# Kernel optimization log

Measured on AMD Instinct MI355X. Metric: run time of the kernel, lower is better.

## Reference

```python
import jax, jax.numpy as jnp
import numpy as np

B, N, HID, H = 2, 2048, 2048, 16
DH = HID // H  # 128


def _rope_tables(n, d, base=10000.0):
    inv_freq = 1.0 / (base ** (np.arange(0, d, 2, dtype=np.float32) / d))
    t = np.arange(n, dtype=np.float32)
    freqs = np.outer(t, inv_freq)                 # [N, d/2]
    emb = np.concatenate([freqs, freqs], axis=-1)  # [N, d]
    return jnp.asarray(np.cos(emb)), jnp.asarray(np.sin(emb))


def setup_inputs() -> dict:
    key = jax.random.key(0)
    k1, k2, k3 = jax.random.split(key, 3)
    std = 1.0 / HID ** 0.5
    cos, sin = _rope_tables(N, DH)
    return {
        "hidden_states": jax.random.normal(k1, (B, N, HID), dtype=jnp.float32),
        "cos": cos,
        "sin": sin,
        "w_qkv": (jax.random.truncated_normal(k2, -2.0, 2.0, (3 * HID, HID), jnp.float32) * std),
        "w_o": (jax.random.truncated_normal(k3, -2.0, 2.0, (HID, HID), jnp.float32) * std),
    }


def _rotate_half(x):
    d = x.shape[-1] // 2
    return jnp.concatenate([-x[..., d:], x[..., :d]], axis=-1)


def reference(hidden_states, cos, sin, w_qkv, w_o):
    b, n, _ = hidden_states.shape
    qkv = (hidden_states @ w_qkv.T).reshape(b, n, 3, H, DH)
    q, k, v = qkv[:, :, 0], qkv[:, :, 1], qkv[:, :, 2]  # [B,N,H,DH]
    c = cos[:, None, :]  # [N,1,DH] broadcasts over heads
    s = sin[:, None, :]
    q = q * c + _rotate_half(q) * s
    k = k * c + _rotate_half(k) * s
    scale = 1.0 / jnp.sqrt(jnp.asarray(DH, q.dtype))
    scores = jnp.einsum("bqhd,bkhd->bhqk", q, k) * scale
    attn = jax.nn.softmax(scores, axis=-1)
    out = jnp.einsum("bhqk,bkhd->bqhd", attn, v).reshape(b, n, HID)
    return out @ w_o.T
```

## Files before the change

kernel.cpp:

```cpp
#include <hip/hip_runtime.h>
#include <math.h>

#define NB 2
#define NN 2048
#define HIDDEN 2048
#define NHEAD 16
#define DHEAD 128

typedef __attribute__((ext_vector_type(8))) short bf16x8;
typedef __attribute__((ext_vector_type(4))) float floatx4;

static __device__ __forceinline__ short f2bf(float f) {
    union { float f; unsigned u; } v; v.f = f;
    unsigned r = v.u + 0x7fffu + ((v.u >> 16) & 1u);
    return (short)(r >> 16);
}
static __device__ __forceinline__ void gload_lds16(const short* g, short* l) {
    __builtin_amdgcn_global_load_lds(
        (const __attribute__((address_space(1))) void*)g,
        (__attribute__((address_space(3))) void*)l, 16, 0, 0);
}

__global__ __launch_bounds__(256) void cast_bf16_3(
    const float* __restrict__ a, const float* __restrict__ b, const float* __restrict__ c,
    short* __restrict__ oa, short* __restrict__ ob, short* __restrict__ oc,
    int n4a, int n4b, int n4c)
{
    int i = blockIdx.x * 256 + threadIdx.x;
    const float* s; short* d; int j;
    if (i < n4a) { s = a; d = oa; j = i; }
    else if (i < n4a + n4b) { s = b; d = ob; j = i - n4a; }
    else if (i < n4a + n4b + n4c) { s = c; d = oc; j = i - n4a - n4b; }
    else return;
    float4 v = ((const float4*)s)[j];
    short4 o;
    o.x = f2bf(v.x); o.y = f2bf(v.y); o.z = f2bf(v.z); o.w = f2bf(v.w);
    ((short4*)d)[j] = o;
}

__global__ __launch_bounds__(512, 2) void gemm_qkv_256(
    const short* __restrict__ A, const short* __restrict__ Bw,
    const float* __restrict__ cosT, const float* __restrict__ sinT,
    short* __restrict__ Qp, short* __restrict__ Kp, short* __restrict__ Vtp)
{
    __shared__ __align__(16) short AB[65536];

    const int tid = threadIdx.x;
    const int w = tid >> 6;
    const int l = tid & 63;
    const int quad = l >> 4;
    const int l15 = l & 15;
    const int wr = w >> 2;
    const int wc = w & 3;
    const int bm = blockIdx.y * 256;
    const int bn = blockIdx.x * 256;
    const int K = HIDDEN;

    const short* src[8];
    int ldst[8];
#pragma unroll
    for (int ld = 0; ld < 2; ++ld) {
        int chunk = ld * 512 + tid;
        int row = chunk >> 3;
        int j = (chunk & 7) ^ (row & 7);
        int coff = j * 8;
        int dbase = chunk * 16;
        src[0 * 2 + ld] = Bw + (size_t)(bn + row) * K + coff;
        src[1 * 2 + ld] = A  + (size_t)(bm + row) * K + coff;
        src[2 * 2 + ld] = A  + (size_t)(bm + 128 + row) * K + coff;
        src[3 * 2 + ld] = Bw + (size_t)(bn + 128 + row) * K + coff;
        ldst[0 * 2 + ld] = 32768 + dbase;
        ldst[1 * 2 + ld] = 0 + dbase;
        ldst[2 * 2 + ld] = 16384 + dbase;
        ldst[3 * 2 + ld] = 32768 + 16384 + dbase;
    }

    const int xj = l15 & 7;
    const int jq0 = ((0 * 4 + quad) ^ xj) * 16;
    const int jq1 = ((1 * 4 + quad) ^ xj) * 16;
    const int arow = (wr * 128 + l15) * 128;
    const int brow = (wc * 16 + l15) * 128;

    floatx4 acc[8][4];
#pragma unroll
    for (int i = 0; i < 8; ++i)
#pragma unroll
        for (int j = 0; j < 4; ++j) acc[i][j] = (floatx4){0.f, 0.f, 0.f, 0.f};

#pragma unroll
    for (int i = 0; i < 8; ++i)
        gload_lds16(src[i], (short*)((char*)AB + ldst[i]));

#define STAGE(i) gload_lds16(src[i] + kpf, (short*)((char*)AB + ldst[i] + so))
#define MFMA(d, x, y) d = __builtin_amdgcn_mfma_f32_16x16x32_bf16(x, y, d, 0, 0, 0)

    const int NT = K / 64;
#pragma unroll 1
    for (int t = 0; t < NT; ++t) {
        const int co = (t & 1) << 16;
        const int so = co ^ 65536;
        int kpf = (t + 1) * 64;
        if (kpf == K) kpf = 0;

        bf16x8 a[4][2], b0[2][2], b1[2][2];

        asm volatile("s_waitcnt vmcnt(2)" ::: "memory");
        __builtin_amdgcn_s_barrier();
#pragma unroll
        for (int m = 0; m < 4; ++m) {
            a[m][0] = *(const bf16x8*)((const char*)AB + co + arow + m * 2048 + jq0);
            a[m][1] = *(const bf16x8*)((const char*)AB + co + arow + m * 2048 + jq1);
        }
#pragma unroll
        for (int n = 0; n < 2; ++n) {
            b0[n][0] = *(const bf16x8*)((const char*)AB + co + 32768 + brow + n * 8192 + jq0);
            b0[n][1] = *(const bf16x8*)((const char*)AB + co + 32768 + brow + n * 8192 + jq1);
        }
        STAGE(0); STAGE(1);
        __builtin_amdgcn_s_setprio(1);
#pragma unroll
        for (int m = 0; m < 4; ++m)
#pragma unroll
            for (int n = 0; n < 2; ++n) {
                MFMA(acc[m][n], a[m][0], b0[n][0]);
                MFMA(acc[m][n], a[m][1], b0[n][1]);
            }
        __builtin_amdgcn_s_setprio(0);

        asm volatile("s_waitcnt vmcnt(2)" ::: "memory");
        __builtin_amdgcn_s_barrier();
#pragma unroll
        for (int n = 0; n < 2; ++n) {
            b1[n][0] = *(const bf16x8*)((const char*)AB + co + 32768 + 16384 + brow + n * 8192 + jq0);
            b1[n][1] = *(const bf16x8*)((const char*)AB + co + 32768 + 16384 + brow + n * 8192 + jq1);
        }
        STAGE(2); STAGE(3);
        __builtin_amdgcn_s_setprio(1);
#pragma unroll
        for (int m = 0; m < 4; ++m)
#pragma unroll
            for (int n = 0; n < 2; ++n) {
                MFMA(acc[m][2 + n], a[m][0], b1[n][0]);
                MFMA(acc[m][2 + n], a[m][1], b1[n][1]);
            }
        __builtin_amdgcn_s_setprio(0);

        __builtin_amdgcn_s_barrier();
#pragma unroll
        for (int m = 0; m < 4; ++m) {
            a[m][0] = *(const bf16x8*)((const char*)AB + co + arow + (4 + m) * 2048 + jq0);
            a[m][1] = *(const bf16x8*)((const char*)AB + co + arow + (4 + m) * 2048 + jq1);
        }
        STAGE(4); STAGE(5);
        __builtin_amdgcn_s_setprio(1);
#pragma unroll
        for (int m = 0; m < 4; ++m)
#pragma unroll
            for (int n = 0; n < 2; ++n) {
                MFMA(acc[4 + m][2 + n], a[m][0], b1[n][0]);
                MFMA(acc[4 + m][2 + n], a[m][1], b1[n][1]);
            }
        __builtin_amdgcn_s_setprio(0);

        __builtin_amdgcn_s_barrier();
        STAGE(6); STAGE(7);
        __builtin_amdgcn_s_setprio(1);
#pragma unroll
        for (int m = 0; m < 4; ++m)
#pragma unroll
            for (int n = 0; n < 2; ++n) {
                MFMA(acc[4 + m][n], a[m][0], b0[n][0]);
                MFMA(acc[4 + m][n], a[m][1], b0[n][1]);
            }
        __builtin_amdgcn_s_setprio(0);
    }
#undef STAGE
#undef MFMA

    asm volatile("s_waitcnt vmcnt(0)" ::: "memory");

    const int bx = blockIdx.x;
    const int which = bx >> 3;
    const int hpair = (bx & 7) * 2;
    const float qsc = (which == 0) ? 0.12751791525f : 1.0f;

#pragma unroll
    for (int m = 0; m < 8; ++m) {
#pragma unroll
        for (int reg = 0; reg < 4; ++reg) {
            int gm = bm + wr * 128 + m * 16 + quad * 4 + reg;
            int b = gm >> 11, nseq = gm & (NN - 1);
            if (which == 2) {
#pragma unroll
                for (int n = 0; n < 4; ++n) {
                    int bh = b * NHEAD + hpair + (n >> 1);
                    int d = (n & 1) * 64 + wc * 16 + l15;
                    Vtp[((size_t)bh * DHEAD + d) * NN + nseq] = f2bf(acc[m][n][reg]);
                }
            } else {
                int d0 = wc * 16 + l15;
                float c = cosT[(size_t)nseq * DHEAD + d0];
                float s = sinT[(size_t)nseq * DHEAD + d0];
#pragma unroll
                for (int hb = 0; hb < 2; ++hb) {
                    int bh = b * NHEAD + hpair + hb;
                    short* dst = (which == 0 ? Qp : Kp) + ((size_t)bh * NN + nseq) * DHEAD;
                    float e0 = acc[m][hb * 2 + 0][reg];
                    float e1 = acc[m][hb * 2 + 1][reg];
                    dst[d0]      = f2bf((e0 * c - e1 * s) * qsc);
                    dst[d0 + 64] = f2bf((e1 * c + e0 * s) * qsc);
                }
            }
        }
    }
}

template <int MODE>
__global__ __launch_bounds__(256) void gemm_bf16_nt(
    const short* __restrict__ A, const short* __restrict__ Bw,
    const float* __restrict__ cosT, const float* __restrict__ sinT,
    short* __restrict__ Qp, short* __restrict__ Kp, short* __restrict__ Vtp,
    float* __restrict__ Cp, int M, int N, int K)
{
    __shared__ __align__(16) short AB[1280 * 8];

    const int tid = threadIdx.x;
    const int w = tid >> 6;
    const int l = tid & 63;
    const int quad = l >> 4;
    const int l15 = l & 15;
    const int bm = blockIdx.y * 128;
    const int bn = blockIdx.x * 128;

    const int wm = (w & 1) * 64;
    const int wn2 = w >> 1;

    const short* gptr[5];
    short* lptr[5];
#pragma unroll
    for (int r5 = 0; r5 < 5; ++r5) {
        int s = r5 * 256 + tid;
        int m = (s < 640) ? s : s - 640;
        int row = m / 5;
        int ch = m - row * 5;
        if (ch == 4) ch = 0;
        gptr[r5] = ((s < 640) ? (A + (size_t)(bm + row) * K)
                              : (Bw + (size_t)(bn + row) * K)) + ch * 8;
        lptr[r5] = &AB[s * 8];
    }

    floatx4 acc[4][4];
#pragma unroll
    for (int i = 0; i < 4; ++i)
#pragma unroll
        for (int j = 0; j < 4; ++j) acc[i][j] = (floatx4){0.f, 0.f, 0.f, 0.f};

    for (int k0 = 0; k0 < K; k0 += 32) {
        __syncthreads();
#pragma unroll
        for (int r5 = 0; r5 < 5; ++r5)
            gload_lds16(gptr[r5] + k0, lptr[r5]);
        __syncthreads();

        bf16x8 af[4], bf[4];
#pragma unroll
        for (int i = 0; i < 4; ++i)
            af[i] = *(const bf16x8*)&AB[((wm + i * 16 + l15) * 5 + quad) * 8];
#pragma unroll
        for (int j = 0; j < 4; ++j) {
            int col = wn2 * 32 + (j & 1) * 16 + ((j >> 1) << 6);
            bf[j] = *(const bf16x8*)&AB[(640 + (col + l15) * 5 + quad) * 8];
        }
#pragma unroll
        for (int i = 0; i < 4; ++i)
#pragma unroll
            for (int j = 0; j < 4; ++j)
                acc[i][j] = __builtin_amdgcn_mfma_f32_16x16x32_bf16(af[i], bf[j], acc[i][j], 0, 0, 0);
    }

    if (MODE == 1) {
#pragma unroll
        for (int i = 0; i < 4; ++i) {
#pragma unroll
            for (int reg = 0; reg < 4; ++reg) {
                int row = bm + wm + i * 16 + quad * 4 + reg;
                float* crow = Cp + (size_t)row * N + bn;
#pragma unroll
                for (int j = 0; j < 4; ++j)
                    crow[wn2 * 32 + (j & 1) * 16 + ((j >> 1) << 6) + l15] = acc[i][j][reg];
            }
        }
    } else {
        const int which = bn >> 11;
        const int head = (bn >> 7) & (NHEAD - 1);
        const float qsc = (which == 0) ? 0.12751791525f : 1.0f;
#pragma unroll
        for (int i = 0; i < 4; ++i) {
#pragma unroll
            for (int reg = 0; reg < 4; ++reg) {
                int m = bm + wm + i * 16 + quad * 4 + reg;
                int b = m >> 11, n = m & (NN - 1);
                int bh = b * NHEAD + head;
                if (which == 2) {
#pragma unroll
                    for (int j = 0; j < 4; ++j) {
                        int d = wn2 * 32 + (j & 1) * 16 + ((j >> 1) << 6) + l15;
                        Vtp[((size_t)bh * DHEAD + d) * NN + n] = f2bf(acc[i][j][reg]);
                    }
                } else {
                    short* dst = (which == 0 ? Qp : Kp) + ((size_t)bh * NN + n) * DHEAD;
#pragma unroll
                    for (int j = 0; j < 2; ++j) {
                        int d0 = wn2 * 32 + j * 16 + l15;
                        float c = cosT[(size_t)n * DHEAD + d0];
                        float s = sinT[(size_t)n * DHEAD + d0];
                        float e0 = acc[i][j][reg], e1 = acc[i][j + 2][reg];
                        dst[d0]      = f2bf((e0 * c - e1 * s) * qsc);
                        dst[d0 + 64] = f2bf((e1 * c + e0 * s) * qsc);
                    }
                }
            }
        }
    }
}

__global__ __launch_bounds__(256, 2) void attn_mfma(
    const short* __restrict__ Qb, const short* __restrict__ Kb,
    const short* __restrict__ Vt, short* __restrict__ AOb)
{
    __shared__ __align__(16) short Ks[64 * 128];
    __shared__ __align__(16) short Vs[128 * 64];
    __shared__ __align__(16) short Ps[4][32][72];

    const int tid = threadIdx.x;
    const int w = tid >> 6;
    const int l = tid & 63;
    const int quad = l >> 4;
    const int l15 = l & 15;
    const int bh = blockIdx.y;
    const int qt = blockIdx.x * 128;

    const short* Qg = Qb + (size_t)bh * NN * DHEAD;
    const short* Kg = Kb + (size_t)bh * NN * DHEAD;
    const short* Vg = Vt + (size_t)bh * DHEAD * NN;

    bf16x8 qf[2][4];
#pragma unroll
    for (int mi = 0; mi < 2; ++mi) {
        const short* qrow = Qg + (size_t)(qt + w * 32 + mi * 16 + l15) * DHEAD + quad * 8;
#pragma unroll
        for (int kc = 0; kc < 4; ++kc) qf[mi][kc] = *(const bf16x8*)(qrow + kc * 32);
    }

    floatx4 of[2][8];
#pragma unroll
    for (int mi = 0; mi < 2; ++mi)
#pragma unroll
        for (int dc = 0; dc < 8; ++dc) of[mi][dc] = (floatx4){0.f, 0.f, 0.f, 0.f};
    float ls[2][4] = {{0.f, 0.f, 0.f, 0.f}, {0.f, 0.f, 0.f, 0.f}};

    for (int kt = 0; kt < NN; kt += 64) {
        __syncthreads();
#pragma unroll
        for (int rr = 0; rr < 4; ++rr) {
            int s = (w * 4 + rr) * 64 + l;
            int row = s >> 4;
            int j = (s & 15) ^ (row & 15);
            gload_lds16(Kg + (size_t)(kt + row) * DHEAD + j * 8, &Ks[s * 8]);
        }
#pragma unroll
        for (int rr = 0; rr < 4; ++rr) {
            int s = (w * 4 + rr) * 64 + l;
            int row = s >> 3;
            int c = (s & 7) ^ (row & 7);
            gload_lds16(Vg + (size_t)row * NN + kt + c * 8, &Vs[s * 8]);
        }
        __syncthreads();

        floatx4 sf[2][4];
#pragma unroll
        for (int n16 = 0; n16 < 4; ++n16) {
            bf16x8 kf[4];
            const short* kbase = &Ks[(n16 * 16 + l15) * 128];
#pragma unroll
            for (int kc = 0; kc < 4; ++kc)
                kf[kc] = *(const bf16x8*)&kbase[((4 * kc + quad) ^ l15) * 8];
#pragma unroll
            for (int mi = 0; mi < 2; ++mi) {
                floatx4 acc = (floatx4){0.f, 0.f, 0.f, 0.f};
#pragma unroll
                for (int kc = 0; kc < 4; ++kc)
                    acc = __builtin_amdgcn_mfma_f32_16x16x32_bf16(qf[mi][kc], kf[kc], acc, 0, 0, 0);
                sf[mi][n16] = acc;
            }
        }

#pragma unroll
        for (int mi = 0; mi < 2; ++mi)
#pragma unroll
            for (int n16 = 0; n16 < 4; ++n16)
#pragma unroll
                for (int r = 0; r < 4; ++r) {
                    float p = exp2f(sf[mi][n16][r]);
                    ls[mi][r] += p;
                    Ps[w][mi * 16 + quad * 4 + r][n16 * 16 + l15] = f2bf(p);
                }

        bf16x8 pa[2][2];
#pragma unroll
        for (int mi = 0; mi < 2; ++mi)
#pragma unroll
            for (int kc = 0; kc < 2; ++kc)
                pa[mi][kc] = *(const bf16x8*)&Ps[w][mi * 16 + l15][kc * 32 + quad * 8];

#pragma unroll
        for (int dc = 0; dc < 8; ++dc) {
            int row = dc * 16 + l15;
#pragma unroll
            for (int kc = 0; kc < 2; ++kc) {
                bf16x8 vf = *(const bf16x8*)&Vs[row * 64 + (((kc * 4 + quad) ^ (row & 7)) * 8)];
#pragma unroll
                for (int mi = 0; mi < 2; ++mi)
                    of[mi][dc] = __builtin_amdgcn_mfma_f32_16x16x32_bf16(
                                     pa[mi][kc], vf, of[mi][dc], 0, 0, 0);
            }
        }
    }

    const int b = bh >> 4, h = bh & (NHEAD - 1);
#pragma unroll
    for (int mi = 0; mi < 2; ++mi)
#pragma unroll
        for (int r = 0; r < 4; ++r) {
            float s = ls[mi][r];
            s += __shfl_xor(s, 1, 64);
            s += __shfl_xor(s, 2, 64);
            s += __shfl_xor(s, 4, 64);
            s += __shfl_xor(s, 8, 64);
            float inv = 1.0f / s;
            int row = qt + w * 32 + mi * 16 + quad * 4 + r;
            short* dst = AOb + ((size_t)(b * NN + row)) * HIDDEN + h * DHEAD;
#pragma unroll
            for (int dc = 0; dc < 8; ++dc)
                dst[dc * 16 + l15] = f2bf(of[mi][dc][r] * inv);
        }
}

extern "C" void kernel_launch(void* const* d_in, const int* in_sizes, int n_in,
                              void* d_out, int out_size, void* d_ws, size_t ws_size,
                              hipStream_t stream)
{
    const float* hs = (const float*)d_in[0];
    const float* cosT = (const float*)d_in[1];
    const float* sinT = (const float*)d_in[2];
    const float* wqkv = (const float*)d_in[3];
    const float* wo = (const float*)d_in[4];
    float* out = (float*)d_out;

    const size_t N_HS = (size_t)NB * NN * HIDDEN;
    const size_t N_WQ = (size_t)3 * HIDDEN * HIDDEN;
    const size_t N_WO = (size_t)HIDDEN * HIDDEN;
    const size_t SZ = (size_t)NB * NHEAD * NN * DHEAD;

    short* Ahs   = (short*)d_ws;
    short* Wqkvb = Ahs + N_HS;
    short* Wob   = Wqkvb + N_WQ;
    short* Qb    = Wob + N_WO;
    short* Kb    = Qb + SZ;
    short* Vtb   = Kb + SZ;
    short* AOb   = Vtb + SZ;

    {
        int n4a = (int)(N_HS / 4), n4b = (int)(N_WQ / 4), n4c = (int)(N_WO / 4);
        int total = n4a + n4b + n4c;
        cast_bf16_3<<<(total + 255) / 256, 256, 0, stream>>>(
            hs, wqkv, wo, Ahs, Wqkvb, Wob, n4a, n4b, n4c);
    }
    {
        dim3 grid(3 * HIDDEN / 256, NB * NN / 256);
        gemm_qkv_256<<<grid, 512, 0, stream>>>(
            Ahs, Wqkvb, cosT, sinT, Qb, Kb, Vtb);
    }
    {
        dim3 grid(NN / 128, NB * NHEAD);
        attn_mfma<<<grid, 256, 0, stream>>>(Qb, Kb, Vtb, AOb);
    }
    {
        dim3 grid(HIDDEN / 128, NB * NN / 128);
        gemm_bf16_nt<1><<<grid, 256, 0, stream>>>(
            AOb, Wob, nullptr, nullptr, nullptr, nullptr, nullptr, out,
            NB * NN, HIDDEN, HIDDEN);
    }
}
```

Baseline: 428.1 us.

## Restructure QKV GEMM prefetch order and barrier placement in main loop

Reorders the global-to-LDS load slots so each quarter-tile stage fetches 64-row strips in the order the MFMA phases consume them. It moves the vmcnt waits to the end of each phase and adds barriers around each prefetch, which gives finer-grained overlap of loads with MFMA work. It also splits the A fragments into separate low and high register sets. The extra barriers and registers could reduce occupancy or add synchronisation stalls.

```diff
diff --git a/kernel.cpp b/kernel.cpp
--- a/kernel.cpp
+++ b/kernel.cpp
@@ -52,34 +52,30 @@
     const int l15 = l & 15;
     const int wr = w >> 2;
     const int wc = w & 3;
+    const int bx = blockIdx.x;
     const int bm = blockIdx.y * 256;
-    const int bn = blockIdx.x * 256;
+    const int bn = bx * 256;
     const int K = HIDDEN;
 
+    const int row64 = tid >> 3;
+    const int jj = (tid & 7) ^ (row64 & 7);
+    const int coff = jj * 8;
     const short* src[8];
     int ldst[8];
-#pragma unroll
-    for (int ld = 0; ld < 2; ++ld) {
-        int chunk = ld * 512 + tid;
-        int row = chunk >> 3;
-        int j = (chunk & 7) ^ (row & 7);
-        int coff = j * 8;
-        int dbase = chunk * 16;
-        src[0 * 2 + ld] = Bw + (size_t)(bn + row) * K + coff;
-        src[1 * 2 + ld] = A  + (size_t)(bm + row) * K + coff;
-        src[2 * 2 + ld] = A  + (size_t)(bm + 128 + row) * K + coff;
-        src[3 * 2 + ld] = Bw + (size_t)(bn + 128 + row) * K + coff;
-        ldst[0 * 2 + ld] = 32768 + dbase;
-        ldst[1 * 2 + ld] = 0 + dbase;
-        ldst[2 * 2 + ld] = 16384 + dbase;
-        ldst[3 * 2 + ld] = 32768 + 16384 + dbase;
-    }
+    src[0] = A  + (size_t)(bm + row64) * K + coff;        ldst[0] = 0     + tid * 16;
+    src[1] = A  + (size_t)(bm + 128 + row64) * K + coff;  ldst[1] = 16384 + tid * 16;
+    src[2] = Bw + (size_t)(bn + row64) * K + coff;        ldst[2] = 32768 + tid * 16;
+    src[3] = Bw + (size_t)(bn + 64 + row64) * K + coff;   ldst[3] = 40960 + tid * 16;
+    src[4] = Bw + (size_t)(bn + 128 + row64) * K + coff;  ldst[4] = 49152 + tid * 16;
+    src[5] = Bw + (size_t)(bn + 192 + row64) * K + coff;  ldst[5] = 57344 + tid * 16;
+    src[6] = A  + (size_t)(bm + 64 + row64) * K + coff;   ldst[6] = 8192  + tid * 16;
+    src[7] = A  + (size_t)(bm + 192 + row64) * K + coff;  ldst[7] = 24576 + tid * 16;
 
     const int xj = l15 & 7;
     const int jq0 = ((0 * 4 + quad) ^ xj) * 16;
     const int jq1 = ((1 * 4 + quad) ^ xj) * 16;
     const int arow = (wr * 128 + l15) * 128;
-    const int brow = (wc * 16 + l15) * 128;
+    const int brow = 32768 + (wc * 16 + l15) * 128;
 
     floatx4 acc[8][4];
 #pragma unroll
@@ -90,6 +86,8 @@
 #pragma unroll
     for (int i = 0; i < 8; ++i)
         gload_lds16(src[i], (short*)((char*)AB + ldst[i]));
+    asm volatile("s_waitcnt vmcnt(4)" ::: "memory");
+    __builtin_amdgcn_s_barrier();
 
 #define STAGE(i) gload_lds16(src[i] + kpf, (short*)((char*)AB + ldst[i] + so))
 #define MFMA(d, x, y) d = __builtin_amdgcn_mfma_f32_16x16x32_bf16(x, y, d, 0, 0, 0)
@@ -102,84 +100,88 @@
         int kpf = (t + 1) * 64;
         if (kpf == K) kpf = 0;
 
-        bf16x8 a[4][2], b0[2][2], b1[2][2];
-
-        asm volatile("s_waitcnt vmcnt(2)" ::: "memory");
-        __builtin_amdgcn_s_barrier();
+        bf16x8 aLo[4][2], aHi[4][2], b01[2][2], b23[2][2];
+
 #pragma unroll
         for (int m = 0; m < 4; ++m) {
-            a[m][0] = *(const bf16x8*)((const char*)AB + co + arow + m * 2048 + jq0);
-            a[m][1] = *(const bf16x8*)((const char*)AB + co + arow + m * 2048 + jq1);
+            aLo[m][0] = *(const bf16x8*)((const char*)AB + co + arow + m * 2048 + jq0);
+            aLo[m][1] = *(const bf16x8*)((const char*)AB + co + arow + m * 2048 + jq1);
         }
 #pragma unroll
         for (int n = 0; n < 2; ++n) {
-            b0[n][0] = *(const bf16x8*)((const char*)AB + co + 32768 + brow + n * 8192 + jq0);
-            b0[n][1] = *(const bf16x8*)((const char*)AB + co + 32768 + brow + n * 8192 + jq1);
+            b01[n][0] = *(const bf16x8*)((const char*)AB + co + brow + n * 8192 + jq0);
+            b01[n][1] = *(const bf16x8*)((const char*)AB + co + brow + n * 8192 + jq1);
         }
         STAGE(0); STAGE(1);
+        __builtin_amdgcn_s_barrier();
         __builtin_amdgcn_s_setprio(1);
 #pragma unroll
         for (int m = 0; m < 4; ++m)
 #pragma unroll
             for (int n = 0; n < 2; ++n) {
-                MFMA(acc[m][n], a[m][0], b0[n][0]);
-                MFMA(acc[m][n], a[m][1], b0[n][1]);
+                MFMA(acc[m][n], aLo[m][0], b01[n][0]);
+                MFMA(acc[m][n], aLo[m][1], b01[n][1]);
             }
         __builtin_amdgcn_s_setprio(0);
-
-        asm volatile("s_waitcnt vmcnt(2)" ::: "memory");
-        __builtin_amdgcn_s_barrier();
+        asm volatile("s_waitcnt vmcnt(4)" ::: "memory");
+        __builtin_amdgcn_s_barrier();
+
 #pragma unroll
         for (int n = 0; n < 2; ++n) {
-            b1[n][0] = *(const bf16x8*)((const char*)AB + co + 32768 + 16384 + brow + n * 8192 + jq0);
-            b1[n][1] = *(const bf16x8*)((const char*)AB + co + 32768 + 16384 + brow + n * 8192 + jq1);
+            b23[n][0] = *(const bf16x8*)((const char*)AB + co + brow + 16384 + n * 8192 + jq0);
+            b23[n][1] = *(const bf16x8*)((const char*)AB + co + brow + 16384 + n * 8192 + jq1);
         }
         STAGE(2); STAGE(3);
+        __builtin_amdgcn_s_barrier();
         __builtin_amdgcn_s_setprio(1);
 #pragma unroll
         for (int m = 0; m < 4; ++m)
 #pragma unroll
             for (int n = 0; n < 2; ++n) {
-                MFMA(acc[m][2 + n], a[m][0], b1[n][0]);
-                MFMA(acc[m][2 + n], a[m][1], b1[n][1]);
+                MFMA(acc[m][2 + n], aLo[m][0], b23[n][0]);
+                MFMA(acc[m][2 + n], aLo[m][1], b23[n][1]);
             }
         __builtin_amdgcn_s_setprio(0);
-
-        __builtin_amdgcn_s_barrier();
+        asm volatile("s_waitcnt vmcnt(4)" ::: "memory");
+        __builtin_amdgcn_s_barrier();
+
 #pragma unroll
         for (int m = 0; m < 4; ++m) {
-            a[m][0] = *(const bf16x8*)((const char*)AB + co + arow + (4 + m) * 2048 + jq0);
-            a[m][1] = *(const bf16x8*)((const char*)AB + co + arow + (4 + m) * 2048 + jq1);
+            aHi[m][0] = *(const bf16x8*)((const char*)AB + co + arow + (4 + m) * 2048 + jq0);
+            aHi[m][1] = *(const bf16x8*)((const char*)AB + co + arow + (4 + m) * 2048 + jq1);
         }
         STAGE(4); STAGE(5);
+        __builtin_amdgcn_s_barrier();
         __builtin_amdgcn_s_setprio(1);
 #pragma unroll
         for (int m = 0; m < 4; ++m)
 #pragma unroll
             for (int n = 0; n < 2; ++n) {
-                MFMA(acc[4 + m][2 + n], a[m][0], b1[n][0]);
-                MFMA(acc[4 + m][2 + n], a[m][1], b1[n][1]);
+                MFMA(acc[4 + m][2 + n], aHi[m][0], b23[n][0]);
+                MFMA(acc[4 + m][2 + n], aHi[m][1], b23[n][1]);
             }
         __builtin_amdgcn_s_setprio(0);
-
-        __builtin_amdgcn_s_barrier();
+        __builtin_amdgcn_s_barrier();
+
         STAGE(6); STAGE(7);
+        __builtin_amdgcn_s_barrier();
         __builtin_amdgcn_s_setprio(1);
 #pragma unroll
         for (int m = 0; m < 4; ++m)
 #pragma unroll
             for (int n = 0; n < 2; ++n) {
-                MFMA(acc[4 + m][n], a[m][0], b0[n][0]);
-                MFMA(acc[4 + m][n], a[m][1], b0[n][1]);
+                MFMA(acc[4 + m][n], aHi[m][0], b01[n][0]);
+                MFMA(acc[4 + m][n], aHi[m][1], b01[n][1]);
             }
         __builtin_amdgcn_s_setprio(0);
+        asm volatile("s_waitcnt vmcnt(4)" ::: "memory");
+        __builtin_amdgcn_s_barrier();
     }
 #undef STAGE
 #undef MFMA
 
     asm volatile("s_waitcnt vmcnt(0)" ::: "memory");
 
-    const int bx = blockIdx.x;
     const int which = bx >> 3;
     const int hpair = (bx & 7) * 2;
     const float qsc = (which == 0) ? 0.12751791525f : 1.0f;
```

Result: slower. 439.8 us (+2.7%).
